# Kernel tuning notes

Hardware: AMD Instinct MI355X
Metric: run time of the kernel (lower is better)

Reference implementation:

```python
import jax, jax.numpy as jnp
import numpy as np

SIZES = [(1362944, 123904), (123904, 11264), (11264, 1024)]  # (n_src, n_tgt) per hop
FANOUT = 10
IN_CH, HID, OUT_CH = 128, 256, 47
BN_EPS = 1e-5


def setup_inputs() -> dict:
    key = jax.random.key(0)
    ks = iter(jax.random.split(key, 64))
    inp = {"x": jax.random.normal(next(ks), (SIZES[0][0], IN_CH), jnp.float32)}
    for i, (ns, nt) in enumerate(SIZES):
        e = nt * FANOUT
        src = jax.random.randint(next(ks), (e,), 0, ns, dtype=jnp.int32)
        tgt = jax.random.randint(next(ks), (e,), 0, nt, dtype=jnp.int32)
        inp[f"ei{i}"] = jnp.stack([src, tgt])  # [2, E]
    dins = [IN_CH, HID, HID]
    for i, din in enumerate(dins):
        inp[f"c{i}_w1"] = jax.random.normal(next(ks), (din, HID), jnp.float32) * (2.0 / din) ** 0.5
        inp[f"c{i}_b1"] = jnp.zeros((HID,), jnp.float32)
        inp[f"c{i}_g"] = jnp.ones((HID,), jnp.float32)
        inp[f"c{i}_be"] = jnp.zeros((HID,), jnp.float32)
        inp[f"c{i}_w2"] = jax.random.normal(next(ks), (HID, HID), jnp.float32) * (2.0 / HID) ** 0.5
        inp[f"c{i}_b2"] = jnp.zeros((HID,), jnp.float32)
    inp["lin1_w"] = jax.random.normal(next(ks), (HID, HID), jnp.float32) * (1.0 / HID) ** 0.5
    inp["lin1_b"] = jnp.zeros((HID,), jnp.float32)
    inp["lin2_w"] = jax.random.normal(next(ks), (HID, OUT_CH), jnp.float32) * (1.0 / HID) ** 0.5
    inp["lin2_b"] = jnp.zeros((OUT_CH,), jnp.float32)
    return inp


def _gin_layer(x, ei, n_tgt, w1, b1, g, be, w2, b2):
    # GINConv(eps=0): h = MLP(x_target + sum_{j->i} x_j)
    x_tgt = x[:n_tgt]
    msg = jax.ops.segment_sum(x[ei[0]], ei[1], num_segments=n_tgt)
    h = x_tgt + msg
    h = h @ w1 + b1
    mu = jnp.mean(h, axis=0)
    var = jnp.var(h, axis=0)  # biased, as in torch BN training mode
    h = (h - mu) * jax.lax.rsqrt(var + BN_EPS) * g + be
    h = jax.nn.relu(h)
    h = jax.nn.relu(h @ w2 + b2)
    return h


def reference(x, ei0, ei1, ei2,
              c0_w1, c0_b1, c0_g, c0_be, c0_w2, c0_b2,
              c1_w1, c1_b1, c1_g, c1_be, c1_w2, c1_b2,
              c2_w1, c2_b1, c2_g, c2_be, c2_w2, c2_b2,
              lin1_w, lin1_b, lin2_w, lin2_b):
    eis = [ei0, ei1, ei2]
    params = [(c0_w1, c0_b1, c0_g, c0_be, c0_w2, c0_b2),
              (c1_w1, c1_b1, c1_g, c1_be, c1_w2, c1_b2),
              (c2_w1, c2_b1, c2_g, c2_be, c2_w2, c2_b2)]
    h = x
    for i, (_, n_tgt) in enumerate(SIZES):
        h = _gin_layer(h, eis[i], n_tgt, *params[i])
    h = jax.nn.relu(h @ lin1_w + lin1_b)
    # dropout(p=0.5) is identity in eval mode
    h = h @ lin2_w + lin2_b
    return jax.nn.log_softmax(h, axis=-1)
```

## Files before the change

### kernel.cpp

```cpp
#include <hip/hip_runtime.h>
#include <cmath>

typedef _Float16 f16;
typedef _Float16 half8 __attribute__((ext_vector_type(8)));
typedef _Float16 half4 __attribute__((ext_vector_type(4)));
typedef float f32x4 __attribute__((ext_vector_type(4)));


__global__ void zero_stats(float* p) { p[blockIdx.x * 256 + threadIdx.x] = 0.f; }

__global__ void zero_i32(int* p, int n) {
    int i = blockIdx.x * 256 + threadIdx.x;
    if (i < n) p[i] = 0;
}

__global__ void wcvt(const float* __restrict__ W, f16* __restrict__ Wt, int K, int N) {
    int i = blockIdx.x * 256 + threadIdx.x;
    if (i < K * N) {
        int k = i / N, n = i - k * N;
        Wt[(size_t)n * K + k] = (f16)W[i];
    }
}

__global__ void lin2t_k(const float* __restrict__ W, float* __restrict__ Wt) {
    int i = blockIdx.x * 256 + threadIdx.x;
    if (i < 256 * 47) {
        int k = i / 47, j = i - k * 47;
        Wt[(size_t)j * 256 + k] = W[i];
    }
}

__device__ __forceinline__ void atomAddF(float* p, float v) { unsafeAtomicAdd(p, v); }


__global__ void fill_adj(const int* __restrict__ src, const int* __restrict__ tgt,
                         int* __restrict__ deg, int* __restrict__ adj, int E) {
    int e = blockIdx.x * 256 + threadIdx.x;
    if (e >= E) return;
    int t = tgt[e];
    int pos = atomicAdd(&deg[t], 1);
    if (pos < 64) adj[(size_t)t * 64 + pos] = src[e];
}


__global__ void gather128(const float* __restrict__ x, const int* __restrict__ deg,
                          const int* __restrict__ adj, f16* __restrict__ h) {
    const int wave = threadIdx.x >> 6, lane = threadIdx.x & 63;
    const int row = blockIdx.x * 4 + wave;
    const int c = lane * 2;
    const float* xr = x + (size_t)row * 128 + c;
    float a0 = xr[0], a1 = xr[1];
    const int n = min(deg[row], 64);
    const int myadj = adj[(size_t)row * 64 + lane];
    for (int j = 0; j < n; ++j) {
        const int s = __shfl(myadj, j);
        const float* xs = x + (size_t)s * 128 + c;
        a0 += xs[0];
        a1 += xs[1];
    }
    f16* hp = h + (size_t)row * 128 + c;
    hp[0] = (f16)a0;
    hp[1] = (f16)a1;
}

__global__ void gather256(const f16* __restrict__ x, const int* __restrict__ deg,
                          const int* __restrict__ adj, f16* __restrict__ h) {
    const int wave = threadIdx.x >> 6, lane = threadIdx.x & 63;
    const int row = blockIdx.x * 4 + wave;
    const int c = lane * 4;
    half4 xv = *(const half4*)(x + (size_t)row * 256 + c);
    float a0 = (float)xv[0], a1 = (float)xv[1], a2 = (float)xv[2], a3 = (float)xv[3];
    const int n = min(deg[row], 64);
    const int myadj = adj[(size_t)row * 64 + lane];
    for (int j = 0; j < n; ++j) {
        const int s = __shfl(myadj, j);
        half4 v = *(const half4*)(x + (size_t)s * 256 + c);
        a0 += (float)v[0];
        a1 += (float)v[1];
        a2 += (float)v[2];
        a3 += (float)v[3];
    }
    half4 o;
    o[0] = (f16)a0;
    o[1] = (f16)a1;
    o[2] = (f16)a2;
    o[3] = (f16)a3;
    *(half4*)(h + (size_t)row * 256 + c) = o;
}

template <bool RELU>
__global__ __launch_bounds__(256) void gemm_bt(const f16* __restrict__ A, const f16* __restrict__ Bt,
                                               const float* __restrict__ bias, f16* __restrict__ C,
                                               int M, int N, int K) {
    constexpr int BM = 64, BN = 64, BK = 32, LP = 40;
    __shared__ f16 sA[BM * LP];
    __shared__ f16 sB[BN * LP];
    const int tid = threadIdx.x;
    const int wave = tid >> 6, lane = tid & 63;
    const int quad = lane >> 4, l16 = lane & 15;
    const int wr = (wave & 1) * 32, wc = (wave >> 1) * 32;
    const int row0 = blockIdx.x * BM, col0 = blockIdx.y * BN;
    const int srow = tid >> 2, soff = (tid & 3) * 8;

    f32x4 acc[2][2] = {};

    for (int k0 = 0; k0 < K; k0 += BK) {
        __syncthreads();
        *(half8*)&sA[srow * LP + soff] =
            *(const half8*)(A + (size_t)(row0 + srow) * K + (k0 + soff));
        *(half8*)&sB[srow * LP + soff] =
            *(const half8*)(Bt + (size_t)(col0 + srow) * K + (k0 + soff));
        __syncthreads();
        half8 af[2], bf[2];
#pragma unroll
        for (int r = 0; r < 2; ++r) af[r] = *(const half8*)&sA[(wr + r * 16 + l16) * LP + quad * 8];
#pragma unroll
        for (int c = 0; c < 2; ++c) bf[c] = *(const half8*)&sB[(wc + c * 16 + l16) * LP + quad * 8];
#pragma unroll
        for (int r = 0; r < 2; ++r)
#pragma unroll
            for (int c = 0; c < 2; ++c)
                acc[r][c] = __builtin_amdgcn_mfma_f32_16x16x32_f16(af[r], bf[c], acc[r][c], 0, 0, 0);
    }

#pragma unroll
    for (int c = 0; c < 2; ++c) {
        const int gcol = col0 + wc + c * 16 + l16;
        const float b = bias[gcol];
#pragma unroll
        for (int r = 0; r < 2; ++r) {
#pragma unroll
            for (int i = 0; i < 4; ++i) {
                const int grow = row0 + wr + r * 16 + quad * 4 + i;
                float v = acc[r][c][i] + b;
                if (RELU) v = fmaxf(v, 0.f);
                C[(size_t)grow * N + gcol] = (f16)v;
            }
        }
    }
}


__global__ void colstats(const f16* __restrict__ h1, int nt, float* __restrict__ colsum,
                         float* __restrict__ colsumsq) {
    const int c = threadIdx.x;
    const int r0 = blockIdx.x * 256;
    const int rend = min(r0 + 256, nt);
    float s = 0.f, ss = 0.f;
    for (int r = r0; r < rend; ++r) {
        float v = (float)h1[(size_t)r * 256 + c];
        s += v;
        ss += v * v;
    }
    atomAddF(&colsum[c], s);
    atomAddF(&colsumsq[c], ss);
}

__global__ void bn_finalize(const float* __restrict__ colsum, const float* __restrict__ colsumsq,
                            const float* __restrict__ g, const float* __restrict__ be, float nt_inv,
                            float* __restrict__ scale, float* __restrict__ shift) {
    int c = threadIdx.x;
    float mu = colsum[c] * nt_inv;
    float var = colsumsq[c] * nt_inv - mu * mu;
    float sc = g[c] * rsqrtf(var + 1e-5f);
    scale[c] = sc;
    shift[c] = be[c] - mu * sc;
}

__global__ void bn_apply(f16* __restrict__ h, int total8, const float* __restrict__ scale,
                         const float* __restrict__ shift) {
    int i = blockIdx.x * 256 + threadIdx.x;
    if (i >= total8) return;
    size_t base = (size_t)i * 8;
    int c = (int)(base & 255);
    half8 v = *(half8*)(h + base);
#pragma unroll
    for (int j = 0; j < 8; ++j) {
        float f = (float)v[j] * scale[c + j] + shift[c + j];
        v[j] = (f16)fmaxf(f, 0.f);
    }
    *(half8*)(h + base) = v;
}

__global__ void head2(const f16* __restrict__ T, const float* __restrict__ w2t,
                      const float* __restrict__ b2, float* __restrict__ out, int rows) {
    const int row = blockIdx.x;
    const int lane = threadIdx.x;
    __shared__ float tr[256];
    for (int i = lane; i < 256; i += 64) tr[i] = (float)T[(size_t)row * 256 + i];
    __syncthreads();
    float d = -1e30f;
    if (lane < 47) {
        const float* wr = w2t + (size_t)lane * 256;
        float dot = 0.f;
        for (int k = 0; k < 256; k += 4) {
            dot += tr[k] * wr[k] + tr[k + 1] * wr[k + 1] + tr[k + 2] * wr[k + 2] +
                   tr[k + 3] * wr[k + 3];
        }
        d = dot + b2[lane];
    }
    float m = d;
    for (int off = 32; off; off >>= 1) m = fmaxf(m, __shfl_xor(m, off));
    float e = (lane < 47) ? expf(d - m) : 0.f;
    float s = e;
    for (int off = 32; off; off >>= 1) s += __shfl_xor(s, off);
    if (lane < 47) out[(size_t)row * 47 + lane] = d - m - logf(s);
}


extern "C" void kernel_launch(void* const* d_in, const int* in_sizes, int n_in, void* d_out,
                              int out_size, void* d_ws, size_t ws_size, hipStream_t stream) {
    const float* x0 = (const float*)d_in[0];
    const int* ei[3] = {(const int*)d_in[1], (const int*)d_in[2], (const int*)d_in[3]};
    const int E[3] = {in_sizes[1] / 2, in_sizes[2] / 2, in_sizes[3] / 2};
    const float* c_w1[3] = {(const float*)d_in[4], (const float*)d_in[10], (const float*)d_in[16]};
    const float* c_b1[3] = {(const float*)d_in[5], (const float*)d_in[11], (const float*)d_in[17]};
    const float* c_g[3] = {(const float*)d_in[6], (const float*)d_in[12], (const float*)d_in[18]};
    const float* c_be[3] = {(const float*)d_in[7], (const float*)d_in[13], (const float*)d_in[19]};
    const float* c_w2[3] = {(const float*)d_in[8], (const float*)d_in[14], (const float*)d_in[20]};
    const float* c_b2[3] = {(const float*)d_in[9], (const float*)d_in[15], (const float*)d_in[21]};
    const float* lin1_w = (const float*)d_in[22];
    const float* lin1_b = (const float*)d_in[23];
    const float* lin2_w = (const float*)d_in[24];
    const float* lin2_b = (const float*)d_in[25];
    float* out = (float*)d_out;

    const int NT[3] = {123904, 11264, 1024};

    char* base = (char*)d_ws;
    size_t off = 0;
    auto take = [&](size_t bytes) -> char* {
        char* p = base + off;
        off = (off + bytes + 255) & ~(size_t)255;
        return p;
    };
    f16* w1t[3];
    w1t[0] = (f16*)take((size_t)256 * 128 * sizeof(f16));
    w1t[1] = (f16*)take((size_t)256 * 256 * sizeof(f16));
    w1t[2] = (f16*)take((size_t)256 * 256 * sizeof(f16));
    f16* w2t[3];
    for (int i = 0; i < 3; ++i) w2t[i] = (f16*)take((size_t)256 * 256 * sizeof(f16));
    f16* lin1t = (f16*)take((size_t)256 * 256 * sizeof(f16));
    float* lin2t_ = (float*)take((size_t)47 * 256 * sizeof(float));
    float* stats = (float*)take(1024 * sizeof(float));
    int* deg = (int*)take((size_t)123904 * sizeof(int));
    int* adj = (int*)take((size_t)123904 * 64 * sizeof(int));
    f16* h0 = (f16*)take((size_t)123904 * 128 * sizeof(f16));
    f16* h1 = (f16*)take((size_t)123904 * 256 * sizeof(f16));
    f16* X1 = (f16*)take((size_t)123904 * 256 * sizeof(f16));
    f16* X2 = (f16*)take((size_t)11264 * 256 * sizeof(f16));
    f16* X3 = (f16*)take((size_t)1024 * 256 * sizeof(f16));
    f16* T = (f16*)take((size_t)1024 * 256 * sizeof(f16));
    (void)ws_size;
    (void)out_size;
    (void)n_in;

    wcvt<<<(128 * 256 + 255) / 256, 256, 0, stream>>>(c_w1[0], w1t[0], 128, 256);
    wcvt<<<256, 256, 0, stream>>>(c_w1[1], w1t[1], 256, 256);
    wcvt<<<256, 256, 0, stream>>>(c_w1[2], w1t[2], 256, 256);
    for (int i = 0; i < 3; ++i) wcvt<<<256, 256, 0, stream>>>(c_w2[i], w2t[i], 256, 256);
    wcvt<<<256, 256, 0, stream>>>(lin1_w, lin1t, 256, 256);
    lin2t_k<<<47, 256, 0, stream>>>(lin2_w, lin2t_);

    auto build_adj = [&](int layer, int nt) {
        zero_i32<<<(nt + 255) / 256, 256, 0, stream>>>(deg, nt);
        fill_adj<<<(E[layer] + 255) / 256, 256, 0, stream>>>(ei[layer], ei[layer] + E[layer], deg,
                                                            adj, E[layer]);
    };

    auto run_post = [&](const f16* w1tp, const float* b1, const float* g, const float* be,
                        const f16* w2tp, const float* b2, f16* Xout, int nt, int K1) {
        gemm_bt<false><<<dim3(nt / 64, 4), 256, 0, stream>>>(h0, w1tp, b1, h1, nt, 256, K1);
        zero_stats<<<2, 256, 0, stream>>>(stats);
        colstats<<<(nt + 255) / 256, 256, 0, stream>>>(h1, nt, stats, stats + 256);
        bn_finalize<<<1, 256, 0, stream>>>(stats, stats + 256, g, be, 1.0f / nt, stats + 512,
                                           stats + 768);
        bn_apply<<<(nt * 256 / 8 + 255) / 256, 256, 0, stream>>>(h1, nt * 256 / 8, stats + 512,
                                                                 stats + 768);
        gemm_bt<true><<<dim3(nt / 64, 4), 256, 0, stream>>>(h1, w2tp, b2, Xout, nt, 256, 256);
    };

    build_adj(0, NT[0]);
    gather128<<<NT[0] / 4, 256, 0, stream>>>(x0, deg, adj, h0);
    run_post(w1t[0], c_b1[0], c_g[0], c_be[0], w2t[0], c_b2[0], X1, NT[0], 128);

    build_adj(1, NT[1]);
    gather256<<<NT[1] / 4, 256, 0, stream>>>(X1, deg, adj, h0);
    run_post(w1t[1], c_b1[1], c_g[1], c_be[1], w2t[1], c_b2[1], X2, NT[1], 256);

    build_adj(2, NT[2]);
    gather256<<<NT[2] / 4, 256, 0, stream>>>(X2, deg, adj, h0);
    run_post(w1t[2], c_b1[2], c_g[2], c_be[2], w2t[2], c_b2[2], X3, NT[2], 256);

    gemm_bt<true><<<dim3(16, 4), 256, 0, stream>>>(X3, lin1t, lin1_b, T, 1024, 256, 256);
    head2<<<1024, 64, 0, stream>>>(T, lin2t_, lin2_b, out, 1024);
}
```

Before: 1.459 ms.

## Add 128x128 LDS-DMA GEMM, batch setup and adjacency build, unroll gathers

Adds a 128x128-tile MFMA GEMM that loads tiles straight into XOR-swizzled shared memory with global_load_lds and uses it for the two larger layers. Merges all weight transposes and degree zeroing into one setup kernel. Builds the adjacency for all three hops in one launch using separate deg/adj regions. Also unrolls the gather loops by four to keep more loads in flight, and halves the rows per colstats block. The aim is fewer launches and more reuse per GEMM tile, at the cost of larger adjacency buffers and more registers per GEMM thread.

```diff
diff --git a/kernel.cpp b/kernel.cpp
--- a/kernel.cpp
+++ b/kernel.cpp
@@ -6,40 +6,68 @@
 typedef _Float16 half4 __attribute__((ext_vector_type(4)));
 typedef float f32x4 __attribute__((ext_vector_type(4)));
 
+__device__ __forceinline__ void atomAddF(float* p, float v) { unsafeAtomicAdd(p, v); }
+
+__device__ __forceinline__ void gload16(const void* g, void* l) {
+    __builtin_amdgcn_global_load_lds((const __attribute__((address_space(1))) void*)g,
+                                     (__attribute__((address_space(3))) void*)l, 16, 0, 0);
+}
+
+struct SetupP {
+    const float* ws[7];
+    f16* wd[7];
+    const float* l2s;
+    float* l2d;
+    int* deg;
+};
+
+__global__ void setup_all(SetupP p) {
+    int i = blockIdx.x * 256 + threadIdx.x;
+    if (i < 32768) {
+        int k = i >> 8, n = i & 255;
+        p.wd[0][(size_t)n * 128 + k] = (f16)p.ws[0][i];
+        return;
+    }
+    i -= 32768;
+    if (i < 6 * 65536) {
+        int m = i >> 16, r = i & 65535;
+        int k = r >> 8, n = r & 255;
+        p.wd[1 + m][(size_t)n * 256 + k] = (f16)p.ws[1 + m][r];
+        return;
+    }
+    i -= 6 * 65536;
+    if (i < 12032) {
+        int k = i / 47, j = i - k * 47;
+        p.l2d[(size_t)j * 256 + k] = p.l2s[i];
+        return;
+    }
+    i -= 12032;
+    if (i < 136192) p.deg[i] = 0;
+}
 
 __global__ void zero_stats(float* p) { p[blockIdx.x * 256 + threadIdx.x] = 0.f; }
 
-__global__ void zero_i32(int* p, int n) {
-    int i = blockIdx.x * 256 + threadIdx.x;
-    if (i < n) p[i] = 0;
-}
-
-__global__ void wcvt(const float* __restrict__ W, f16* __restrict__ Wt, int K, int N) {
-    int i = blockIdx.x * 256 + threadIdx.x;
-    if (i < K * N) {
-        int k = i / N, n = i - k * N;
-        Wt[(size_t)n * K + k] = (f16)W[i];
-    }
-}
-
-__global__ void lin2t_k(const float* __restrict__ W, float* __restrict__ Wt) {
-    int i = blockIdx.x * 256 + threadIdx.x;
-    if (i < 256 * 47) {
-        int k = i / 47, j = i - k * 47;
-        Wt[(size_t)j * 256 + k] = W[i];
-    }
-}
-
-__device__ __forceinline__ void atomAddF(float* p, float v) { unsafeAtomicAdd(p, v); }
-
-
-__global__ void fill_adj(const int* __restrict__ src, const int* __restrict__ tgt,
-                         int* __restrict__ deg, int* __restrict__ adj, int E) {
+__global__ void fill_all(const int* __restrict__ e0, const int* __restrict__ e1,
+                         const int* __restrict__ e2, int E0, int E1, int E2, int* __restrict__ deg,
+                         int* __restrict__ adj) {
     int e = blockIdx.x * 256 + threadIdx.x;
-    if (e >= E) return;
+    const int *src, *tgt;
+    int* d;
+    int* a;
+    if (e < E0) {
+        src = e0; tgt = e0 + E0; d = deg; a = adj;
+    } else if (e < E0 + E1) {
+        e -= E0;
+        src = e1; tgt = e1 + E1; d = deg + 123904; a = adj + (size_t)123904 * 64;
+    } else if (e < E0 + E1 + E2) {
+        e -= E0 + E1;
+        src = e2; tgt = e2 + E2; d = deg + 135168; a = adj + (size_t)135168 * 64;
+    } else {
+        return;
+    }
     int t = tgt[e];
-    int pos = atomicAdd(&deg[t], 1);
-    if (pos < 64) adj[(size_t)t * 64 + pos] = src[e];
+    int pos = atomicAdd(&d[t], 1);
+    if (pos < 64) a[(size_t)t * 64 + pos] = src[e];
 }
 
 
@@ -52,11 +80,24 @@
     float a0 = xr[0], a1 = xr[1];
     const int n = min(deg[row], 64);
     const int myadj = adj[(size_t)row * 64 + lane];
-    for (int j = 0; j < n; ++j) {
-        const int s = __shfl(myadj, j);
-        const float* xs = x + (size_t)s * 128 + c;
-        a0 += xs[0];
-        a1 += xs[1];
+    int j = 0;
+    for (; j + 4 <= n; j += 4) {
+        int s0 = __shfl(myadj, j), s1 = __shfl(myadj, j + 1);
+        int s2 = __shfl(myadj, j + 2), s3 = __shfl(myadj, j + 3);
+        const float* p0 = x + (size_t)s0 * 128 + c;
+        const float* p1 = x + (size_t)s1 * 128 + c;
+        const float* p2 = x + (size_t)s2 * 128 + c;
+        const float* p3 = x + (size_t)s3 * 128 + c;
+        float b00 = p0[0], b01 = p0[1], b10 = p1[0], b11 = p1[1];
+        float b20 = p2[0], b21 = p2[1], b30 = p3[0], b31 = p3[1];
+        a0 += (b00 + b10) + (b20 + b30);
+        a1 += (b01 + b11) + (b21 + b31);
+    }
+    for (; j < n; ++j) {
+        int s = __shfl(myadj, j);
+        const float* p = x + (size_t)s * 128 + c;
+        a0 += p[0];
+        a1 += p[1];
     }
     f16* hp = h + (size_t)row * 128 + c;
     hp[0] = (f16)a0;
@@ -72,8 +113,21 @@
     float a0 = (float)xv[0], a1 = (float)xv[1], a2 = (float)xv[2], a3 = (float)xv[3];
     const int n = min(deg[row], 64);
     const int myadj = adj[(size_t)row * 64 + lane];
-    for (int j = 0; j < n; ++j) {
-        const int s = __shfl(myadj, j);
+    int j = 0;
+    for (; j + 4 <= n; j += 4) {
+        int s0 = __shfl(myadj, j), s1 = __shfl(myadj, j + 1);
+        int s2 = __shfl(myadj, j + 2), s3 = __shfl(myadj, j + 3);
+        half4 v0 = *(const half4*)(x + (size_t)s0 * 256 + c);
+        half4 v1 = *(const half4*)(x + (size_t)s1 * 256 + c);
+        half4 v2 = *(const half4*)(x + (size_t)s2 * 256 + c);
+        half4 v3 = *(const half4*)(x + (size_t)s3 * 256 + c);
+        a0 += ((float)v0[0] + (float)v1[0]) + ((float)v2[0] + (float)v3[0]);
+        a1 += ((float)v0[1] + (float)v1[1]) + ((float)v2[1] + (float)v3[1]);
+        a2 += ((float)v0[2] + (float)v1[2]) + ((float)v2[2] + (float)v3[2]);
+        a3 += ((float)v0[3] + (float)v1[3]) + ((float)v2[3] + (float)v3[3]);
+    }
+    for (; j < n; ++j) {
+        int s = __shfl(myadj, j);
         half4 v = *(const half4*)(x + (size_t)s * 256 + c);
         a0 += (float)v[0];
         a1 += (float)v[1];
@@ -86,6 +140,74 @@
     o[2] = (f16)a2;
     o[3] = (f16)a3;
     *(half4*)(h + (size_t)row * 256 + c) = o;
+}
+
+template <bool RELU>
+__global__ __launch_bounds__(256) void gemm128(const f16* __restrict__ A, const f16* __restrict__ Bt,
+                                               const float* __restrict__ bias, f16* __restrict__ C,
+                                               int M, int N, int K) {
+    __shared__ __attribute__((aligned(16))) f16 sA[128 * 32];
+    __shared__ __attribute__((aligned(16))) f16 sB[128 * 32];
+    const int tid = threadIdx.x;
+    const int wave = tid >> 6, lane = tid & 63;
+    const int quad = lane >> 4, l16 = lane & 15;
+    const int wr = (wave & 1) * 64, wc = (wave >> 1) * 64;
+    const int row0 = blockIdx.x * 128, col0 = blockIdx.y * 128;
+
+    const int i0 = tid, i1 = tid + 256;
+    const int r0s = i0 >> 2, c0s = (i0 & 3) ^ ((r0s >> 1) & 3);
+    const int r1s = i1 >> 2, c1s = (i1 & 3) ^ ((r1s >> 1) & 3);
+    const f16* ga0 = A + (size_t)(row0 + r0s) * K + c0s * 8;
+    const f16* ga1 = A + (size_t)(row0 + r1s) * K + c1s * 8;
+    const f16* gb0 = Bt + (size_t)(col0 + r0s) * K + c0s * 8;
+    const f16* gb1 = Bt + (size_t)(col0 + r1s) * K + c1s * 8;
+    f16* la0 = &sA[i0 * 8];
+    f16* la1 = &sA[i1 * 8];
+    f16* lb0 = &sB[i0 * 8];
+    f16* lb1 = &sB[i1 * 8];
+
+    f32x4 acc[4][4] = {};
+
+    for (int k0 = 0; k0 < K; k0 += 32) {
+        __syncthreads();
+        gload16(ga0 + k0, la0);
+        gload16(ga1 + k0, la1);
+        gload16(gb0 + k0, lb0);
+        gload16(gb1 + k0, lb1);
+        __syncthreads();
+        half8 af[4], bf[4];
+#pragma unroll
+        for (int r = 0; r < 4; ++r) {
+            const int ar = wr + r * 16 + l16;
+            af[r] = *(const half8*)&sA[ar * 32 + ((quad ^ ((ar >> 1) & 3)) * 8)];
+        }
+#pragma unroll
+        for (int c = 0; c < 4; ++c) {
+            const int br = wc + c * 16 + l16;
+            bf[c] = *(const half8*)&sB[br * 32 + ((quad ^ ((br >> 1) & 3)) * 8)];
+        }
+#pragma unroll
+        for (int r = 0; r < 4; ++r)
+#pragma unroll
+            for (int c = 0; c < 4; ++c)
+                acc[r][c] = __builtin_amdgcn_mfma_f32_16x16x32_f16(af[r], bf[c], acc[r][c], 0, 0, 0);
+    }
+
+#pragma unroll
+    for (int c = 0; c < 4; ++c) {
+        const int gcol = col0 + wc + c * 16 + l16;
+        const float b = bias[gcol];
+#pragma unroll
+        for (int r = 0; r < 4; ++r) {
+#pragma unroll
+            for (int i = 0; i < 4; ++i) {
+                const int grow = row0 + wr + r * 16 + quad * 4 + i;
+                float v = acc[r][c][i] + b;
+                if (RELU) v = fmaxf(v, 0.f);
+                C[(size_t)grow * N + gcol] = (f16)v;
+            }
+        }
+    }
 }
 
 template <bool RELU>
@@ -144,8 +266,8 @@
 __global__ void colstats(const f16* __restrict__ h1, int nt, float* __restrict__ colsum,
                          float* __restrict__ colsumsq) {
     const int c = threadIdx.x;
-    const int r0 = blockIdx.x * 256;
-    const int rend = min(r0 + 256, nt);
+    const int r0 = blockIdx.x * 128;
+    const int rend = min(r0 + 128, nt);
     float s = 0.f, ss = 0.f;
     for (int r = r0; r < rend; ++r) {
         float v = (float)h1[(size_t)r * 256 + c];
@@ -243,8 +365,8 @@
     f16* lin1t = (f16*)take((size_t)256 * 256 * sizeof(f16));
     float* lin2t_ = (float*)take((size_t)47 * 256 * sizeof(float));
     float* stats = (float*)take(1024 * sizeof(float));
-    int* deg = (int*)take((size_t)123904 * sizeof(int));
-    int* adj = (int*)take((size_t)123904 * 64 * sizeof(int));
+    int* deg = (int*)take((size_t)136192 * sizeof(int));
+    int* adj = (int*)take((size_t)136192 * 64 * sizeof(int));
     f16* h0 = (f16*)take((size_t)123904 * 128 * sizeof(f16));
     f16* h1 = (f16*)take((size_t)123904 * 256 * sizeof(f16));
     f16* X1 = (f16*)take((size_t)123904 * 256 * sizeof(f16));
@@ -255,42 +377,61 @@
     (void)out_size;
     (void)n_in;
 
-    wcvt<<<(128 * 256 + 255) / 256, 256, 0, stream>>>(c_w1[0], w1t[0], 128, 256);
-    wcvt<<<256, 256, 0, stream>>>(c_w1[1], w1t[1], 256, 256);
-    wcvt<<<256, 256, 0, stream>>>(c_w1[2], w1t[2], 256, 256);
-    for (int i = 0; i < 3; ++i) wcvt<<<256, 256, 0, stream>>>(c_w2[i], w2t[i], 256, 256);
-    wcvt<<<256, 256, 0, stream>>>(lin1_w, lin1t, 256, 256);
-    lin2t_k<<<47, 256, 0, stream>>>(lin2_w, lin2t_);
-
-    auto build_adj = [&](int layer, int nt) {
-        zero_i32<<<(nt + 255) / 256, 256, 0, stream>>>(deg, nt);
-        fill_adj<<<(E[layer] + 255) / 256, 256, 0, stream>>>(ei[layer], ei[layer] + E[layer], deg,
-                                                            adj, E[layer]);
-    };
-
-    auto run_post = [&](const f16* w1tp, const float* b1, const float* g, const float* be,
-                        const f16* w2tp, const float* b2, f16* Xout, int nt, int K1) {
-        gemm_bt<false><<<dim3(nt / 64, 4), 256, 0, stream>>>(h0, w1tp, b1, h1, nt, 256, K1);
+    int* deg_l[3] = {deg, deg + 123904, deg + 135168};
+    int* adj_l[3] = {adj, adj + (size_t)123904 * 64, adj + (size_t)135168 * 64};
+
+    SetupP sp;
+    sp.ws[0] = c_w1[0];
+    sp.ws[1] = c_w1[1];
+    sp.ws[2] = c_w1[2];
+    sp.ws[3] = c_w2[0];
+    sp.ws[4] = c_w2[1];
+    sp.ws[5] = c_w2[2];
+    sp.ws[6] = lin1_w;
+    sp.wd[0] = w1t[0];
+    sp.wd[1] = w1t[1];
+    sp.wd[2] = w1t[2];
+    sp.wd[3] = w2t[0];
+    sp.wd[4] = w2t[1];
+    sp.wd[5] = w2t[2];
+    sp.wd[6] = lin1t;
+    sp.l2s = lin2_w;
+    sp.l2d = lin2t_;
+    sp.deg = deg;
+    setup_all<<<(574208 + 255) / 256, 256, 0, stream>>>(sp);
+
+    fill_all<<<(E[0] + E[1] + E[2] + 255) / 256, 256, 0, stream>>>(ei[0], ei[1], ei[2], E[0], E[1],
+                                                                  E[2], deg, adj);
+
+    auto bn_mid = [&](const float* g, const float* be, int nt) {
         zero_stats<<<2, 256, 0, stream>>>(stats);
-        colstats<<<(nt + 255) / 256, 256, 0, stream>>>(h1, nt, stats, stats + 256);
+        colstats<<<(nt + 127) / 128, 256, 0, stream>>>(h1, nt, stats, stats + 256);
         bn_finalize<<<1, 256, 0, stream>>>(stats, stats + 256, g, be, 1.0f / nt, stats + 512,
                                            stats + 768);
         bn_apply<<<(nt * 256 / 8 + 255) / 256, 256, 0, stream>>>(h1, nt * 256 / 8, stats + 512,
                                                                  stats + 768);
-        gemm_bt<true><<<dim3(nt / 64, 4), 256, 0, stream>>>(h1, w2tp, b2, Xout, nt, 256, 256);
     };
 
-    build_adj(0, NT[0]);
-    gather128<<<NT[0] / 4, 256, 0, stream>>>(x0, deg, adj, h0);
-    run_post(w1t[0], c_b1[0], c_g[0], c_be[0], w2t[0], c_b2[0], X1, NT[0], 128);
-
-    build_adj(1, NT[1]);
-    gather256<<<NT[1] / 4, 256, 0, stream>>>(X1, deg, adj, h0);
-    run_post(w1t[1], c_b1[1], c_g[1], c_be[1], w2t[1], c_b2[1], X2, NT[1], 256);
-
-    build_adj(2, NT[2]);
-    gather256<<<NT[2] / 4, 256, 0, stream>>>(X2, deg, adj, h0);
-    run_post(w1t[2], c_b1[2], c_g[2], c_be[2], w2t[2], c_b2[2], X3, NT[2], 256);
+    gather128<<<NT[0] / 4, 256, 0, stream>>>(x0, deg_l[0], adj_l[0], h0);
+    gemm128<false><<<dim3(NT[0] / 128, 2), 256, 0, stream>>>(h0, w1t[0], c_b1[0], h1, NT[0], 256,
+                                                             128);
+    bn_mid(c_g[0], c_be[0], NT[0]);
+    gemm128<true><<<dim3(NT[0] / 128, 2), 256, 0, stream>>>(h1, w2t[0], c_b2[0], X1, NT[0], 256,
+                                                            256);
+
+    gather256<<<NT[1] / 4, 256, 0, stream>>>(X1, deg_l[1], adj_l[1], h0);
+    gemm128<false><<<dim3(NT[1] / 128, 2), 256, 0, stream>>>(h0, w1t[1], c_b1[1], h1, NT[1], 256,
+                                                             256);
+    bn_mid(c_g[1], c_be[1], NT[1]);
+    gemm128<true><<<dim3(NT[1] / 128, 2), 256, 0, stream>>>(h1, w2t[1], c_b2[1], X2, NT[1], 256,
+                                                            256);
+
+    gather256<<<NT[2] / 4, 256, 0, stream>>>(X2, deg_l[2], adj_l[2], h0);
+    gemm_bt<false><<<dim3(NT[2] / 64, 4), 256, 0, stream>>>(h0, w1t[2], c_b1[2], h1, NT[2], 256,
+                                                            256);
+    bn_mid(c_g[2], c_be[2], NT[2]);
+    gemm_bt<true><<<dim3(NT[2] / 64, 4), 256, 0, stream>>>(h1, w2t[2], c_b2[2], X3, NT[2], 256,
+                                                           256);
 
     gemm_bt<true><<<dim3(16, 4), 256, 0, stream>>>(X3, lin1t, lin1_b, T, 1024, 256, 256);
     head2<<<1024, 64, 0, stream>>>(T, lin2t_, lin2_b, out, 1024);
```

Result: faster. 1.302 ms (-10.8%).
